# Performance work log

Measured on AMD Instinct MI355X. Metric: run time of the kernel, lower is better.

## Reference

```python
import jax, jax.numpy as jnp
import numpy as np

B, H, D, M = 128, 8, 256, 8192
K, RANK = 32, 16
EPS = 1e-8


def setup_inputs() -> dict:
    key = jax.random.key(0)
    ks = jax.random.split(key, 8)
    s = 0.02
    inv_sqrt_d = 1.0 / np.sqrt(D).astype(np.float32)
    return {
        "psi": jax.random.normal(ks[0], (B, D, 2), jnp.float32),
        "u_real": jax.random.normal(ks[1], (M, D), jnp.float32) * s,
        "u_imag": jax.random.normal(ks[2], (M, D), jnp.float32) * s,
        "w_real": jax.random.normal(ks[3], (M, D), jnp.float32) * s,
        "w_imag": jax.random.normal(ks[4], (M, D), jnp.float32) * s,
        "s_logit": jnp.full((M,), -2.0, jnp.float32),
        # orthogonal init approximated by scaled gaussian (init only, not math)
        "probe_real": jax.random.normal(ks[5], (H, D, D), jnp.float32) * inv_sqrt_d,
        "probe_imag": jax.random.normal(ks[6], (H, D, D), jnp.float32) * inv_sqrt_d,
        "k": K,
        "rank": RANK,
    }


def reference(psi, u_real, u_imag, w_real, w_imag, s_logit,
              probe_real, probe_imag, k, rank):
    temperature = 1.0
    # ---- project_query: q_h = (Wr + i Wi) psi,  psi: [B,d,2] -> q: [B,H,d] complex parts
    pr, pi = psi[..., 0], psi[..., 1]
    qr = jnp.einsum('hij,bj->bhi', probe_real, pr) - jnp.einsum('hij,bj->bhi', probe_imag, pi)
    qi = jnp.einsum('hij,bj->bhi', probe_real, pi) + jnp.einsum('hij,bj->bhi', probe_imag, pr)
    # ---- effect_directions: L2-normalize complex u over d
    nrm = jnp.sqrt(jnp.clip(jnp.sum(u_real**2 + u_imag**2, axis=-1, keepdims=True), EPS))
    ur, ui = u_real / nrm, u_imag / nrm
    # ---- probe scores: |u_m^dag q|^2 * sigma(s_m) / tau  -> [B,H,M]
    ip_r = jnp.einsum('md,bhd->bhm', ur, qr) + jnp.einsum('md,bhd->bhm', ui, qi)
    ip_i = jnp.einsum('md,bhd->bhm', ur, qi) - jnp.einsum('md,bhd->bhm', ui, qr)
    scores = jax.nn.sigmoid(s_logit)[None, None, :] * (ip_r**2 + ip_i**2) / max(temperature, 1e-6)
    # ---- top-k select + gather directions/values, weight by sqrt(score)
    topk_vals, topk_idx = jax.lax.top_k(scores, k)          # [B,H,k]
    u_c = (ur + 1j * ui).astype(jnp.complex64)[topk_idx]    # [B,H,k,d]
    w_c = (w_real + 1j * w_imag).astype(jnp.complex64)[topk_idx]
    weights = jnp.sqrt(jnp.clip(topk_vals, 0.0))[..., None] # [B,H,k,1]
    u_mat = jnp.swapaxes(u_c * weights, -1, -2)             # [B,H,d,k]
    w_mat = jnp.swapaxes(w_c * weights, -1, -2)             # [B,H,d,k]
    # ---- batched complex QR, pad/truncate Q to rank cols
    Q, _ = jnp.linalg.qr(u_mat)                             # [B,H,d,min(d,k)]
    cols = Q.shape[-1]
    if cols < rank:
        Q = jnp.concatenate([Q, jnp.zeros(Q.shape[:-1] + (rank - cols,), Q.dtype)], axis=-1)
    elif cols > rank:
        Q = Q[..., :rank]
    # ---- align values: V = Q[:, :eff] * diag(Q^H w)
    coeff = jnp.einsum('bhdr,bhdk->bhrk', Q.conj(), w_c.swapaxes(-1, -2) * 0 + w_mat)  # [B,H,rank,k]
    eff = min(rank, k)
    diag = jnp.diagonal(coeff[..., :eff, :eff], axis1=-2, axis2=-1)  # [B,H,eff]
    V = Q[..., :eff] * diag[..., None, :]
    if eff < rank:
        V = jnp.concatenate([V, jnp.zeros(V.shape[:-1] + (rank - eff,), V.dtype)], axis=-1)
    U_re = jnp.stack([Q.real, Q.imag], axis=-1)  # [B,H,d,rank,2]
    V_re = jnp.stack([V.real, V.imag], axis=-1)  # [B,H,d,rank,2]
    return (U_re, V_re)
```

## Files before the change

### kernel.cpp

```cpp
#include <hip/hip_runtime.h>
#include <math.h>

#define BB 128
#define HH 8
#define DD 256
#define MM 8192
#define BH (BB*HH)
#define RANK 16

typedef __attribute__((ext_vector_type(8))) short bf16x8;
typedef __attribute__((ext_vector_type(4))) float f32x4;

__device__ inline unsigned short f2bf(float f) {
  unsigned x = __float_as_uint(f);
  unsigned r = x + 0x7FFFu + ((x >> 16) & 1u);
  return (unsigned short)(r >> 16);
}
__device__ inline float bf2f(unsigned short u) {
  return __uint_as_float(((unsigned)u) << 16);
}

__global__ __launch_bounds__(256) void k_q(
    const float* __restrict__ psi, const float* __restrict__ probe_r,
    const float* __restrict__ probe_i, float* __restrict__ qr, float* __restrict__ qi) {
  __shared__ float2 ps0[DD];
  __shared__ float2 ps1[DD];
  int b0 = blockIdx.x * 2;
  int h  = blockIdx.y;
  int i  = threadIdx.x;
  ps0[i] = ((const float2*)psi)[(size_t)b0 * DD + i];
  ps1[i] = ((const float2*)psi)[(size_t)(b0 + 1) * DD + i];
  __syncthreads();
  const float* rr = probe_r + ((size_t)h * DD + i) * DD;
  const float* ri = probe_i + ((size_t)h * DD + i) * DD;
  float a0r = 0.f, a0i = 0.f, a1r = 0.f, a1i = 0.f;
  for (int j = 0; j < DD; j += 4) {
    float4 xr = *(const float4*)(rr + j);
    float4 xi = *(const float4*)(ri + j);
    float2 p0 = ps0[j+0], p1 = ps0[j+1], p2 = ps0[j+2], p3 = ps0[j+3];
    a0r += xr.x*p0.x - xi.x*p0.y;  a0i += xr.x*p0.y + xi.x*p0.x;
    a0r += xr.y*p1.x - xi.y*p1.y;  a0i += xr.y*p1.y + xi.y*p1.x;
    a0r += xr.z*p2.x - xi.z*p2.y;  a0i += xr.z*p2.y + xi.z*p2.x;
    a0r += xr.w*p3.x - xi.w*p3.y;  a0i += xr.w*p3.y + xi.w*p3.x;
    float2 s0 = ps1[j+0], s1 = ps1[j+1], s2 = ps1[j+2], s3 = ps1[j+3];
    a1r += xr.x*s0.x - xi.x*s0.y;  a1i += xr.x*s0.y + xi.x*s0.x;
    a1r += xr.y*s1.x - xi.y*s1.y;  a1i += xr.y*s1.y + xi.y*s1.x;
    a1r += xr.z*s2.x - xi.z*s2.y;  a1i += xr.z*s2.y + xi.z*s2.x;
    a1r += xr.w*s3.x - xi.w*s3.y;  a1i += xr.w*s3.y + xi.w*s3.x;
  }
  size_t o0 = ((size_t)(b0    ) * HH + h) * DD + i;
  size_t o1 = ((size_t)(b0 + 1) * HH + h) * DD + i;
  qr[o0] = a0r; qi[o0] = a0i;
  qr[o1] = a1r; qi[o1] = a1i;
}

__global__ __launch_bounds__(256) void k_norm(
    const float* __restrict__ u_r, const float* __restrict__ u_i,
    const float* __restrict__ s_logit, float* __restrict__ inv_nrm,
    float* __restrict__ fac) {
  int m = blockIdx.x * 4 + (threadIdx.x >> 6);
  int lane = threadIdx.x & 63;
  const float4* a = (const float4*)(u_r + (size_t)m * DD);
  const float4* b = (const float4*)(u_i + (size_t)m * DD);
  float4 x = a[lane], y = b[lane];
  float s = x.x*x.x + x.y*x.y + x.z*x.z + x.w*x.w
          + y.x*y.x + y.y*y.y + y.z*y.z + y.w*y.w;
  for (int off = 32; off; off >>= 1) s += __shfl_down(s, off);
  if (lane == 0) {
    float inv = 1.0f / sqrtf(fmaxf(s, 1e-8f));
    inv_nrm[m] = inv;
    float sig = 1.0f / (1.0f + expf(-s_logit[m]));
    fac[m] = sig * inv * inv;
  }
}

__global__ __launch_bounds__(256) void k_convA(
    const float* __restrict__ qr, const float* __restrict__ qi,
    unsigned short* __restrict__ Ap) {
  int bh = blockIdx.x, d = threadIdx.x;
  float xr = qr[(size_t)bh*DD + d], xi = qi[(size_t)bh*DD + d];
  unsigned short hr = f2bf(xr), hi_ = f2bf(xi);
  unsigned short* r0 = Ap + (size_t)(2*bh) * 512;
  unsigned short* r1 = r0 + 512;
  r0[d] = hr;  r0[256+d] = hi_;
  r1[d] = hi_; r1[256+d] = hr ^ 0x8000u;
}

__global__ __launch_bounds__(256) void k_convB(
    const float* __restrict__ u_r, const float* __restrict__ u_i,
    unsigned short* __restrict__ Bp) {
  int m = blockIdx.x, d = threadIdx.x;
  unsigned short* r = Bp + (size_t)m * 512;
  r[d]     = f2bf(u_r[(size_t)m*DD + d]);
  r[256+d] = f2bf(u_i[(size_t)m*DD + d]);
}

__global__ __launch_bounds__(256, 4) void k_gemm(
    const unsigned short* __restrict__ Ap,
    const unsigned short* __restrict__ Bp,
    const float* __restrict__ fac,
    unsigned short* __restrict__ sc) {
  __shared__ __align__(16) unsigned short SMEM[16384];
  unsigned short* As = SMEM;
  unsigned short* Bs = SMEM + 8192;
  int tid  = threadIdx.x;
  int lane = tid & 63, wid = tid >> 6;
  int wm = wid >> 1, wn = wid & 1;
  int a_row0 = blockIdx.y * 128;
  int b_row0 = blockIdx.x * 128;

  int st_r0 = tid >> 3;
  int st_kc = tid & 7;
  int st_slot = (st_kc ^ (st_r0 & 7)) * 16;

  int arow = lane & 15;
  int fr_g = lane >> 4;
  int r7   = lane & 7;
  const char* Abase = (const char*)As + (wm*64 + arow) * 128;
  const char* Bbase = (const char*)Bs + (wn*64 + arow) * 128;

  f32x4 acc[4][4];
#pragma unroll
  for (int i = 0; i < 4; ++i)
#pragma unroll
    for (int j = 0; j < 4; ++j) acc[i][j] = (f32x4){0.f,0.f,0.f,0.f};

  int4 ra[4], rb[4];
  {
    const unsigned short* pa = Ap + (size_t)(a_row0 + st_r0)*512 + 8*st_kc;
    const unsigned short* pb = Bp + (size_t)(b_row0 + st_r0)*512 + 8*st_kc;
#pragma unroll
    for (int i = 0; i < 4; ++i) {
      ra[i] = *(const int4*)(pa + (size_t)i*32*512);
      rb[i] = *(const int4*)(pb + (size_t)i*32*512);
    }
  }
  const int NT = 8;
  for (int t = 0; t < NT; ++t) {
    __syncthreads();
#pragma unroll
    for (int i = 0; i < 4; ++i) {
      *(int4*)((char*)As + (st_r0 + 32*i)*128 + st_slot) = ra[i];
      *(int4*)((char*)Bs + (st_r0 + 32*i)*128 + st_slot) = rb[i];
    }
    __syncthreads();
    if (t + 1 < NT) {
      int k0 = (t + 1) * 64;
      const unsigned short* pa = Ap + (size_t)(a_row0 + st_r0)*512 + k0 + 8*st_kc;
      const unsigned short* pb = Bp + (size_t)(b_row0 + st_r0)*512 + k0 + 8*st_kc;
#pragma unroll
      for (int i = 0; i < 4; ++i) {
        ra[i] = *(const int4*)(pa + (size_t)i*32*512);
        rb[i] = *(const int4*)(pb + (size_t)i*32*512);
      }
    }
#pragma unroll
    for (int ks = 0; ks < 2; ++ks) {
      int slot = ((ks*4 + fr_g) ^ r7) * 16;
      bf16x8 a[4], b[4];
#pragma unroll
      for (int fm = 0; fm < 4; ++fm) a[fm] = *(const bf16x8*)(Abase + fm*2048 + slot);
#pragma unroll
      for (int fn = 0; fn < 4; ++fn) b[fn] = *(const bf16x8*)(Bbase + fn*2048 + slot);
#pragma unroll
      for (int fm = 0; fm < 4; ++fm)
#pragma unroll
        for (int fn = 0; fn < 4; ++fn)
          acc[fm][fn] = __builtin_amdgcn_mfma_f32_16x16x32_bf16(a[fm], b[fn], acc[fm][fn], 0, 0, 0);
    }
  }
  __syncthreads();
  const int LP = 136;
  int lr0 = wm*32 + 2*(lane >> 4);
  int lc0 = wn*64 + (lane & 15);
  float fv[4];
#pragma unroll
  for (int fn = 0; fn < 4; ++fn)
    fv[fn] = fac[blockIdx.x*128 + lc0 + fn*16];
#pragma unroll
  for (int fm = 0; fm < 4; ++fm) {
#pragma unroll
    for (int fn = 0; fn < 4; ++fn) {
      f32x4 c = acc[fm][fn];
      float s0 = fv[fn]*(c.x*c.x + c.y*c.y);
      float s1 = fv[fn]*(c.z*c.z + c.w*c.w);
      SMEM[(lr0 + fm*8    ) * LP + lc0 + fn*16] = f2bf(s0);
      SMEM[(lr0 + fm*8 + 1) * LP + lc0 + fn*16] = f2bf(s1);
    }
  }
  __syncthreads();
  {
    int row = tid >> 2;
    int seg = tid & 3;
    unsigned short* dst = sc + (size_t)(blockIdx.y*64 + row) * MM
                             + blockIdx.x*128 + seg*32;
    const unsigned short* src = SMEM + row*LP + seg*32;
#pragma unroll
    for (int c4 = 0; c4 < 4; ++c4)
      *(int4*)(dst + c4*8) = *(const int4*)(src + c4*8);
  }
}

__global__ __launch_bounds__(256) void k_top32(
    const unsigned short* __restrict__ sc, int* __restrict__ cand) {
  __shared__ unsigned long long wtop[128];
  int bh = blockIdx.x, half = blockIdx.y;
  int tid = threadIdx.x, lane = tid & 63, w = tid >> 6;
  const unsigned short* row = sc + (size_t)bh * MM + half*4096;
  unsigned long long v[16];
#pragma unroll
  for (int j = 0; j < 16; ++j) {
    int idx = j*256 + tid;
    unsigned bits = ((unsigned)row[idx]) << 16;
    v[j] = (((unsigned long long)bits) << 32) | (unsigned)(4095 - idx);
  }
  for (int r = 0; r < 32; ++r) {
    unsigned long long bk = v[0]; int bj = 0;
#pragma unroll
    for (int j = 1; j < 16; ++j) if (v[j] > bk) { bk = v[j]; bj = j; }
    unsigned long long mx = bk;
    for (int off = 32; off; off >>= 1) {
      unsigned long long o = __shfl_xor(mx, off);
      if (o > mx) mx = o;
    }
    if (bk == mx && mx != 0ull) {
#pragma unroll
      for (int j = 0; j < 16; ++j) if (j == bj) v[j] = 0ull;
    }
    if (lane == 0) wtop[w*32 + r] = mx;
  }
  __syncthreads();
  if (w == 0) {
    unsigned long long a = wtop[lane], b = wtop[64 + lane];
    for (int r = 0; r < 32; ++r) {
      unsigned long long bk = (a > b) ? a : b;
      int which = (a > b) ? 0 : 1;
      unsigned long long mx = bk;
      for (int off = 32; off; off >>= 1) {
        unsigned long long o = __shfl_xor(mx, off);
        if (o > mx) mx = o;
      }
      if (bk == mx && mx != 0ull) { if (which == 0) a = 0ull; else b = 0ull; }
      if (lane == 0) {
        int idx = 4095 - (int)(mx & 0xFFFFFFFFull);
        cand[bh*64 + half*32 + r] = half*4096 + idx;
      }
    }
  }
}

__global__ __launch_bounds__(256) void k_exact(
    const float* __restrict__ qr, const float* __restrict__ qi,
    const float* __restrict__ u_r, const float* __restrict__ u_i,
    const float* __restrict__ fac, const int* __restrict__ cand,
    float* __restrict__ topv, int* __restrict__ topi) {
  __shared__ float qrs[DD], qis[DD];
  __shared__ unsigned long long keys[64];
  int bh = blockIdx.x, tid = threadIdx.x, lane = tid & 63, w = tid >> 6;
  qrs[tid] = qr[(size_t)bh*DD + tid];
  qis[tid] = qi[(size_t)bh*DD + tid];
  __syncthreads();
  float4 xr = *(const float4*)&qrs[lane*4];
  float4 xi = *(const float4*)&qis[lane*4];
  for (int c = 0; c < 16; ++c) {
    int ci = w*16 + c;
    int m = cand[bh*64 + ci];
    float4 a = *(const float4*)(u_r + (size_t)m*DD + lane*4);
    float4 b = *(const float4*)(u_i + (size_t)m*DD + lane*4);
    float pr = a.x*xr.x + a.y*xr.y + a.z*xr.z + a.w*xr.w
             + b.x*xi.x + b.y*xi.y + b.z*xi.z + b.w*xi.w;
    float pi2 = a.x*xi.x + a.y*xi.y + a.z*xi.z + a.w*xi.w
              - (b.x*xr.x + b.y*xr.y + b.z*xr.z + b.w*xr.w);
    for (int off = 32; off; off >>= 1) {
      pr  += __shfl_down(pr, off);
      pi2 += __shfl_down(pi2, off);
    }
    if (lane == 0) {
      float s = fac[m] * (pr*pr + pi2*pi2);
      keys[ci] = (((unsigned long long)__float_as_uint(s)) << 32)
               | (unsigned)(MM - 1 - m);
    }
  }
  __syncthreads();
  if (w == 0) {
    unsigned long long k = keys[lane];
    for (int r = 0; r < 16; ++r) {
      unsigned long long mx = k;
      for (int off = 32; off; off >>= 1) {
        unsigned long long o = __shfl_xor(mx, off);
        if (o > mx) mx = o;
      }
      if (k == mx && mx != 0ull) k = 0ull;
      if (lane == 0) {
        topv[bh*16 + r] = __uint_as_float((unsigned)(mx >> 32));
        topi[bh*16 + r] = MM - 1 - (int)(mx & 0xFFFFFFFFull);
      }
    }
  }
}

__global__ __launch_bounds__(256) void k_qr(
    const float* __restrict__ u_r, const float* __restrict__ u_i,
    const float* __restrict__ inv_nrm,
    const float* __restrict__ w_r, const float* __restrict__ w_i,
    const float* __restrict__ topv, const int* __restrict__ topi,
    float* __restrict__ out) {
  __shared__ float Ar[DD][17];
  __shared__ float Ai[DD][17];
  __shared__ float pwR[16][16], pwI[16][16];
  __shared__ float wvR[16], wvI[16];
  __shared__ float redS[4];
  __shared__ int   idxs[16];
  __shared__ float fA[16], fW[16];
  __shared__ float tauR[16], tauI[16];
  __shared__ float dgR[16], dgI[16];

  int bh = blockIdx.x;
  int tid = threadIdx.x;
  int d = tid;
  if (tid < 16) {
    int id = topi[bh*16 + tid];
    idxs[tid] = id;
    float w = sqrtf(fmaxf(topv[bh*16 + tid], 0.f));
    fW[tid] = w;
    fA[tid] = w * inv_nrm[id];
  }
  __syncthreads();
  for (int j = 0; j < 16; ++j) {
    float f = fA[j];
    size_t base = (size_t)idxs[j] * DD + d;
    Ar[d][j] = u_r[base] * f;
    Ai[d][j] = u_i[base] * f;
  }
  __syncthreads();

  for (int j = 0; j < 16; ++j) {
    float ar = Ar[d][j], ai = Ai[d][j];
    float xn2 = (d > j) ? (ar*ar + ai*ai) : 0.f;
    for (int off = 32; off; off >>= 1) xn2 += __shfl_down(xn2, off);
    int lane = tid & 63, wv_ = tid >> 6;
    if (lane == 0) redS[wv_] = xn2;
    __syncthreads();
    xn2 = redS[0] + redS[1] + redS[2] + redS[3];
    float alr = Ar[j][j], ali = Ai[j][j];
    float taur, taui, scr, sci;
    if (xn2 == 0.f && ali == 0.f) {
      taur = 0.f; taui = 0.f; scr = 0.f; sci = 0.f;
    } else {
      float nrm  = sqrtf(alr*alr + ali*ali + xn2);
      float beta = (alr >= 0.f) ? -nrm : nrm;
      taur = (beta - alr) / beta;
      taui = -ali / beta;
      float dr = alr - beta, di = ali;
      float den = dr*dr + di*di;
      scr = dr / den; sci = -di / den;
    }
    __syncthreads();
    if (d > j) {
      float vr = ar*scr - ai*sci;
      float vi = ar*sci + ai*scr;
      Ar[d][j] = vr; Ai[d][j] = vi;
    } else if (d == j) {
      Ar[d][j] = 1.f; Ai[d][j] = 0.f;
      tauR[j] = taur; tauI[j] = taui;
    }
    __syncthreads();
    int c16 = tid & 15, seg = tid >> 4;
    float wr = 0.f, wi = 0.f;
    if (c16 > j) {
      for (int i2 = 0; i2 < 16; ++i2) {
        int dd = seg*16 + i2;
        if (dd >= j) {
          float vr = Ar[dd][j], vi = Ai[dd][j];
          float br = Ar[dd][c16], bi = Ai[dd][c16];
          wr += vr*br + vi*bi;
          wi += vr*bi - vi*br;
        }
      }
    }
    pwR[seg][c16] = wr; pwI[seg][c16] = wi;
    __syncthreads();
    if (tid < 16) {
      float swr = 0.f, swi = 0.f;
      for (int s = 0; s < 16; ++s) { swr += pwR[s][tid]; swi += pwI[s][tid]; }
      wvR[tid] = swr; wvI[tid] = swi;
    }
    __syncthreads();
    if (d >= j) {
      float vr = Ar[d][j], vi = Ai[d][j];
      float tr = taur*vr + taui*vi;
      float ti = taur*vi - taui*vr;
      for (int cc = j+1; cc < 16; ++cc) {
        float wr2 = wvR[cc], wi2 = wvI[cc];
        Ar[d][cc] -= tr*wr2 - ti*wi2;
        Ai[d][cc] -= tr*wi2 + ti*wr2;
      }
    }
    __syncthreads();
  }

  for (int i = 15; i >= 0; --i) {
    float tr = tauR[i], ti = tauI[i];
    int c16 = tid & 15, seg = tid >> 4;
    float wr = 0.f, wi = 0.f;
    if (c16 > i) {
      for (int i2 = 0; i2 < 16; ++i2) {
        int dd = seg*16 + i2;
        if (dd >= i) {
          float vr = Ar[dd][i], vi = Ai[dd][i];
          float br = Ar[dd][c16], bi = Ai[dd][c16];
          wr += vr*br + vi*bi;
          wi += vr*bi - vi*br;
        }
      }
    }
    pwR[seg][c16] = wr; pwI[seg][c16] = wi;
    __syncthreads();
    if (tid < 16) {
      float swr = 0.f, swi = 0.f;
      for (int s = 0; s < 16; ++s) { swr += pwR[s][tid]; swi += pwI[s][tid]; }
      wvR[tid] = swr; wvI[tid] = swi;
    }
    __syncthreads();
    float vr = Ar[d][i], vi = Ai[d][i];
    if (d >= i) {
      float tvr = tr*vr - ti*vi;
      float tvi = tr*vi + ti*vr;
      for (int cc = i+1; cc < 16; ++cc) {
        Ar[d][cc] -= tvr*wvR[cc] - tvi*wvI[cc];
        Ai[d][cc] -= tvr*wvI[cc] + tvi*wvR[cc];
      }
      if (d > i) {
        Ar[d][i] = -(tr*vr - ti*vi);
        Ai[d][i] = -(tr*vi + ti*vr);
      } else {
        Ar[d][i] = 1.f - tr;
        Ai[d][i] = -ti;
      }
    } else {
      Ar[d][i] = 0.f;
      Ai[d][i] = 0.f;
    }
    __syncthreads();
  }

  {
    int r16 = tid & 15, seg = tid >> 4;
    float fr = fW[r16];
    size_t rowb = (size_t)idxs[r16] * DD + seg*16;
    float sr = 0.f, si = 0.f;
    for (int i2 = 0; i2 < 16; ++i2) {
      int dd = seg*16 + i2;
      float wr2 = w_r[rowb + i2] * fr;
      float wi2 = w_i[rowb + i2] * fr;
      float qr2 = Ar[dd][r16], qi2 = Ai[dd][r16];
      sr += qr2*wr2 + qi2*wi2;
      si += qr2*wi2 - qi2*wr2;
    }
    pwR[seg][r16] = sr; pwI[seg][r16] = si;
  }
  __syncthreads();
  if (tid < 16) {
    float sr = 0.f, si = 0.f;
    for (int s = 0; s < 16; ++s) { sr += pwR[s][tid]; si += pwI[s][tid]; }
    dgR[tid] = sr; dgI[tid] = si;
  }
  __syncthreads();
  size_t baseU = ((size_t)bh * DD + d) * 32;
  size_t baseV = (size_t)BH * DD * 32 + baseU;
  float4* oU = (float4*)(out + baseU);
  float4* oV = (float4*)(out + baseV);
#pragma unroll
  for (int r = 0; r < 16; r += 2) {
    float q0r = Ar[d][r],   q0i = Ai[d][r];
    float q1r = Ar[d][r+1], q1i = Ai[d][r+1];
    oU[r >> 1] = make_float4(q0r, q0i, q1r, q1i);
    float v0r = q0r*dgR[r]   - q0i*dgI[r];
    float v0i = q0r*dgI[r]   + q0i*dgR[r];
    float v1r = q1r*dgR[r+1] - q1i*dgI[r+1];
    float v1i = q1r*dgI[r+1] + q1i*dgR[r+1];
    oV[r >> 1] = make_float4(v0r, v0i, v1r, v1i);
  }
}

extern "C" void kernel_launch(void* const* d_in, const int* in_sizes, int n_in,
                              void* d_out, int out_size, void* d_ws, size_t ws_size,
                              hipStream_t stream) {
  (void)in_sizes; (void)n_in; (void)out_size; (void)ws_size;
  const float* psi     = (const float*)d_in[0];
  const float* u_r     = (const float*)d_in[1];
  const float* u_i     = (const float*)d_in[2];
  const float* w_r     = (const float*)d_in[3];
  const float* w_i     = (const float*)d_in[4];
  const float* s_logit = (const float*)d_in[5];
  const float* probe_r = (const float*)d_in[6];
  const float* probe_i = (const float*)d_in[7];

  float* ws = (float*)d_ws;
  float*          qr      = ws;
  float*          qi      = ws + 262144;
  float*          inv_nrm = ws + 524288;
  float*          fac     = ws + 532480;
  float*          topv    = ws + 540672;
  int*            topi    = (int*)(ws + 557056);
  int*            cand    = (int*)(ws + 573440);
  unsigned short* Ap      = (unsigned short*)(ws + 638976);
  unsigned short* Bp      = (unsigned short*)(ws + 1163264);
  unsigned short* sc      = (unsigned short*)(ws + 3260416);
  float* out = (float*)d_out;

  hipLaunchKernelGGL(k_q,     dim3(BB/2, HH), dim3(256), 0, stream,
                     psi, probe_r, probe_i, qr, qi);
  hipLaunchKernelGGL(k_norm,  dim3(MM/4),     dim3(256), 0, stream,
                     u_r, u_i, s_logit, inv_nrm, fac);
  hipLaunchKernelGGL(k_convA, dim3(BH),       dim3(256), 0, stream, qr, qi, Ap);
  hipLaunchKernelGGL(k_convB, dim3(MM),       dim3(256), 0, stream, u_r, u_i, Bp);
  hipLaunchKernelGGL(k_gemm,  dim3(64, 16),   dim3(256), 0, stream,
                     Ap, Bp, fac, sc);
  hipLaunchKernelGGL(k_top32, dim3(BH, 2),    dim3(256), 0, stream, sc, cand);
  hipLaunchKernelGGL(k_exact, dim3(BH),       dim3(256), 0, stream,
                     qr, qi, u_r, u_i, fac, cand, topv, topi);
  hipLaunchKernelGGL(k_qr,    dim3(BH),       dim3(256), 0, stream,
                     u_r, u_i, inv_nrm, w_r, w_i, topv, topi, out);
}
```

Before: 448.3 us.

## Keep Householder QR columns in registers and reduce with wave shuffles

The batched complex QR kernel now keeps each thread's row of the 256x16 matrix in registers instead of a padded shared-memory array. Column inner products are computed with wave-level shuffle reductions plus a small per-wave shared buffer. This cuts the barriers per Householder step and removes the 16-segment partial-sum passes, lowering LDS traffic and sync cost. It adds register pressure and many more shuffles, and the dynamic column index is resolved through unrolled compare-select loops.

```diff
diff --git a/kernel.cpp b/kernel.cpp
--- a/kernel.cpp
+++ b/kernel.cpp
@@ -305,19 +305,18 @@
     const float* __restrict__ w_r, const float* __restrict__ w_i,
     const float* __restrict__ topv, const int* __restrict__ topi,
     float* __restrict__ out) {
-  __shared__ float Ar[DD][17];
-  __shared__ float Ai[DD][17];
-  __shared__ float pwR[16][16], pwI[16][16];
-  __shared__ float wvR[16], wvI[16];
   __shared__ float redS[4];
+  __shared__ float alphaSh[2];
+  __shared__ float pw[4][32];
+  __shared__ float tauSh[16][2];
   __shared__ int   idxs[16];
   __shared__ float fA[16], fW[16];
-  __shared__ float tauR[16], tauI[16];
-  __shared__ float dgR[16], dgI[16];
 
   int bh = blockIdx.x;
   int tid = threadIdx.x;
   int d = tid;
+  int lane = tid & 63, wv = tid >> 6;
+
   if (tid < 16) {
     int id = topi[bh*16 + tid];
     idxs[tid] = id;
@@ -326,23 +325,27 @@
     fA[tid] = w * inv_nrm[id];
   }
   __syncthreads();
+
+  float Ar[16], Ai[16];
+#pragma unroll
   for (int j = 0; j < 16; ++j) {
     float f = fA[j];
     size_t base = (size_t)idxs[j] * DD + d;
-    Ar[d][j] = u_r[base] * f;
-    Ai[d][j] = u_i[base] * f;
-  }
-  __syncthreads();
+    Ar[j] = u_r[base] * f;
+    Ai[j] = u_i[base] * f;
+  }
 
   for (int j = 0; j < 16; ++j) {
-    float ar = Ar[d][j], ai = Ai[d][j];
+    float ar = 0.f, ai = 0.f;
+#pragma unroll
+    for (int c = 0; c < 16; ++c) if (c == j) { ar = Ar[c]; ai = Ai[c]; }
     float xn2 = (d > j) ? (ar*ar + ai*ai) : 0.f;
     for (int off = 32; off; off >>= 1) xn2 += __shfl_down(xn2, off);
-    int lane = tid & 63, wv_ = tid >> 6;
-    if (lane == 0) redS[wv_] = xn2;
+    if (lane == 0) redS[wv] = xn2;
+    if (d == j) { alphaSh[0] = ar; alphaSh[1] = ai; }
     __syncthreads();
     xn2 = redS[0] + redS[1] + redS[2] + redS[3];
-    float alr = Ar[j][j], ali = Ai[j][j];
+    float alr = alphaSh[0], ali = alphaSh[1];
     float taur, taui, scr, sci;
     if (xn2 == 0.f && ali == 0.f) {
       taur = 0.f; taui = 0.f; scr = 0.f; sci = 0.f;
@@ -355,125 +358,96 @@
       float den = dr*dr + di*di;
       scr = dr / den; sci = -di / den;
     }
-    __syncthreads();
-    if (d > j) {
-      float vr = ar*scr - ai*sci;
-      float vi = ar*sci + ai*scr;
-      Ar[d][j] = vr; Ai[d][j] = vi;
-    } else if (d == j) {
-      Ar[d][j] = 1.f; Ai[d][j] = 0.f;
-      tauR[j] = taur; tauI[j] = taui;
-    }
-    __syncthreads();
-    int c16 = tid & 15, seg = tid >> 4;
-    float wr = 0.f, wi = 0.f;
-    if (c16 > j) {
-      for (int i2 = 0; i2 < 16; ++i2) {
-        int dd = seg*16 + i2;
-        if (dd >= j) {
-          float vr = Ar[dd][j], vi = Ai[dd][j];
-          float br = Ar[dd][c16], bi = Ai[dd][c16];
-          wr += vr*br + vi*bi;
-          wi += vr*bi - vi*br;
-        }
-      }
-    }
-    pwR[seg][c16] = wr; pwI[seg][c16] = wi;
-    __syncthreads();
-    if (tid < 16) {
-      float swr = 0.f, swi = 0.f;
-      for (int s = 0; s < 16; ++s) { swr += pwR[s][tid]; swi += pwI[s][tid]; }
-      wvR[tid] = swr; wvI[tid] = swi;
-    }
-    __syncthreads();
-    if (d >= j) {
-      float vr = Ar[d][j], vi = Ai[d][j];
-      float tr = taur*vr + taui*vi;
-      float ti = taur*vi - taui*vr;
-      for (int cc = j+1; cc < 16; ++cc) {
-        float wr2 = wvR[cc], wi2 = wvI[cc];
-        Ar[d][cc] -= tr*wr2 - ti*wi2;
-        Ai[d][cc] -= tr*wi2 + ti*wr2;
-      }
-    }
-    __syncthreads();
+    if (tid == 0) { tauSh[j][0] = taur; tauSh[j][1] = taui; }
+    float vr, vi;
+    if (d > j)       { vr = ar*scr - ai*sci; vi = ar*sci + ai*scr; }
+    else if (d == j) { vr = 1.f; vi = 0.f; }
+    else             { vr = 0.f; vi = 0.f; }
+#pragma unroll
+    for (int c = 0; c < 16; ++c) if (c == j) { Ar[c] = vr; Ai[c] = vi; }
+#pragma unroll
+    for (int c = 0; c < 16; ++c) if (c > j) {
+      float lr = vr*Ar[c] + vi*Ai[c];
+      float li = vr*Ai[c] - vi*Ar[c];
+      for (int off = 32; off; off >>= 1) {
+        lr += __shfl_down(lr, off);
+        li += __shfl_down(li, off);
+      }
+      if (lane == 0) { pw[wv][2*c] = lr; pw[wv][2*c+1] = li; }
+    }
+    __syncthreads();
+    float tr = taur*vr + taui*vi;
+    float ti = taur*vi - taui*vr;
+#pragma unroll
+    for (int c = 0; c < 16; ++c) if (c > j) {
+      float wcr = pw[0][2*c] + pw[1][2*c] + pw[2][2*c] + pw[3][2*c];
+      float wci = pw[0][2*c+1] + pw[1][2*c+1] + pw[2][2*c+1] + pw[3][2*c+1];
+      Ar[c] -= tr*wcr - ti*wci;
+      Ai[c] -= tr*wci + ti*wcr;
+    }
   }
 
   for (int i = 15; i >= 0; --i) {
-    float tr = tauR[i], ti = tauI[i];
-    int c16 = tid & 15, seg = tid >> 4;
-    float wr = 0.f, wi = 0.f;
-    if (c16 > i) {
-      for (int i2 = 0; i2 < 16; ++i2) {
-        int dd = seg*16 + i2;
-        if (dd >= i) {
-          float vr = Ar[dd][i], vi = Ai[dd][i];
-          float br = Ar[dd][c16], bi = Ai[dd][c16];
-          wr += vr*br + vi*bi;
-          wi += vr*bi - vi*br;
-        }
-      }
-    }
-    pwR[seg][c16] = wr; pwI[seg][c16] = wi;
-    __syncthreads();
-    if (tid < 16) {
-      float swr = 0.f, swi = 0.f;
-      for (int s = 0; s < 16; ++s) { swr += pwR[s][tid]; swi += pwI[s][tid]; }
-      wvR[tid] = swr; wvI[tid] = swi;
-    }
-    __syncthreads();
-    float vr = Ar[d][i], vi = Ai[d][i];
-    if (d >= i) {
-      float tvr = tr*vr - ti*vi;
-      float tvi = tr*vi + ti*vr;
-      for (int cc = i+1; cc < 16; ++cc) {
-        Ar[d][cc] -= tvr*wvR[cc] - tvi*wvI[cc];
-        Ai[d][cc] -= tvr*wvI[cc] + tvi*wvR[cc];
-      }
-      if (d > i) {
-        Ar[d][i] = -(tr*vr - ti*vi);
-        Ai[d][i] = -(tr*vi + ti*vr);
-      } else {
-        Ar[d][i] = 1.f - tr;
-        Ai[d][i] = -ti;
-      }
-    } else {
-      Ar[d][i] = 0.f;
-      Ai[d][i] = 0.f;
-    }
-    __syncthreads();
-  }
-
-  {
-    int r16 = tid & 15, seg = tid >> 4;
-    float fr = fW[r16];
-    size_t rowb = (size_t)idxs[r16] * DD + seg*16;
-    float sr = 0.f, si = 0.f;
-    for (int i2 = 0; i2 < 16; ++i2) {
-      int dd = seg*16 + i2;
-      float wr2 = w_r[rowb + i2] * fr;
-      float wi2 = w_i[rowb + i2] * fr;
-      float qr2 = Ar[dd][r16], qi2 = Ai[dd][r16];
-      sr += qr2*wr2 + qi2*wi2;
-      si += qr2*wi2 - qi2*wr2;
-    }
-    pwR[seg][r16] = sr; pwI[seg][r16] = si;
-  }
-  __syncthreads();
-  if (tid < 16) {
-    float sr = 0.f, si = 0.f;
-    for (int s = 0; s < 16; ++s) { sr += pwR[s][tid]; si += pwI[s][tid]; }
-    dgR[tid] = sr; dgI[tid] = si;
-  }
-  __syncthreads();
+    __syncthreads();
+    float taur = tauSh[i][0], taui = tauSh[i][1];
+    float vr = 0.f, vi = 0.f;
+#pragma unroll
+    for (int c = 0; c < 16; ++c) if (c == i) { vr = Ar[c]; vi = Ai[c]; }
+#pragma unroll
+    for (int c = 0; c < 16; ++c) if (c > i) {
+      float lr = vr*Ar[c] + vi*Ai[c];
+      float li = vr*Ai[c] - vi*Ar[c];
+      for (int off = 32; off; off >>= 1) {
+        lr += __shfl_down(lr, off);
+        li += __shfl_down(li, off);
+      }
+      if (lane == 0) { pw[wv][2*c] = lr; pw[wv][2*c+1] = li; }
+    }
+    __syncthreads();
+    float tvr = taur*vr - taui*vi;
+    float tvi = taur*vi + taui*vr;
+#pragma unroll
+    for (int c = 0; c < 16; ++c) if (c > i) {
+      float wcr = pw[0][2*c] + pw[1][2*c] + pw[2][2*c] + pw[3][2*c];
+      float wci = pw[0][2*c+1] + pw[1][2*c+1] + pw[2][2*c+1] + pw[3][2*c+1];
+      Ar[c] -= tvr*wcr - tvi*wci;
+      Ai[c] -= tvr*wci + tvi*wcr;
+    }
+    float er = (d == i) ? 1.f : 0.f;
+#pragma unroll
+    for (int c = 0; c < 16; ++c) if (c == i) { Ar[c] = er - tvr; Ai[c] = -tvi; }
+  }
+
+  __syncthreads();
+#pragma unroll
+  for (int r = 0; r < 16; ++r) {
+    size_t base = (size_t)idxs[r] * DD + d;
+    float wr2 = w_r[base], wi2 = w_i[base];
+    float lr = Ar[r]*wr2 + Ai[r]*wi2;
+    float li = Ar[r]*wi2 - Ai[r]*wr2;
+    for (int off = 32; off; off >>= 1) {
+      lr += __shfl_down(lr, off);
+      li += __shfl_down(li, off);
+    }
+    if (lane == 0) { pw[wv][2*r] = lr; pw[wv][2*r+1] = li; }
+  }
+  __syncthreads();
+  float dgR[16], dgI[16];
+#pragma unroll
+  for (int r = 0; r < 16; ++r) {
+    float f = fW[r];
+    dgR[r] = (pw[0][2*r] + pw[1][2*r] + pw[2][2*r] + pw[3][2*r]) * f;
+    dgI[r] = (pw[0][2*r+1] + pw[1][2*r+1] + pw[2][2*r+1] + pw[3][2*r+1]) * f;
+  }
+
   size_t baseU = ((size_t)bh * DD + d) * 32;
   size_t baseV = (size_t)BH * DD * 32 + baseU;
   float4* oU = (float4*)(out + baseU);
   float4* oV = (float4*)(out + baseV);
 #pragma unroll
   for (int r = 0; r < 16; r += 2) {
-    float q0r = Ar[d][r],   q0i = Ai[d][r];
-    float q1r = Ar[d][r+1], q1i = Ai[d][r+1];
+    float q0r = Ar[r],   q0i = Ai[r];
+    float q1r = Ar[r+1], q1i = Ai[r+1];
     oU[r >> 1] = make_float4(q0r, q0i, q1r, q1i);
     float v0r = q0r*dgR[r]   - q0i*dgI[r];
     float v0i = q0r*dgI[r]   + q0i*dgR[r];
```

New measurement: 551.7 us. +23.1%, slower.
